# Optimization experiments

Hardware: AMD Instinct MI355X
Metric: run time of the kernel (lower is better)

The kernel has to match this reference:

```python
import jax, jax.numpy as jnp
import numpy as np

D_MODEL = 1024
N_HEAD = 16
T = 2048
HEAD = D_MODEL // N_HEAD  # 64
RANKS = [32, 16, 8, 8]
BLOCKS = [2048, 1024, 512, 256]  # seq_len // 2**i ('default')
OFFS = np.cumsum([0] + RANKS)


def setup_inputs() -> dict:
    key = jax.random.key(0)
    k0, k1, k2 = jax.random.split(key, 3)
    s = 0.02
    x = jax.random.normal(k0, (1, T, D_MODEL), dtype=jnp.float32)
    W_attn = jax.random.normal(k1, (D_MODEL, 3 * D_MODEL), dtype=jnp.float32) * s
    b_attn = jnp.zeros((3 * D_MODEL,), dtype=jnp.float32)
    W_proj = jax.random.normal(k2, (D_MODEL, D_MODEL), dtype=jnp.float32) * s
    b_proj = jnp.zeros((D_MODEL,), dtype=jnp.float32)
    return {"x": x, "W_attn": W_attn, "b_attn": b_attn, "W_proj": W_proj, "b_proj": b_proj}


def reference(x, W_attn, b_attn, W_proj, b_proj):
    B = x.shape[0]
    qkv = x @ W_attn + b_attn  # (B,T,3*D)
    q, k, v = jnp.split(qkv, 3, axis=-1)
    # (B,H,T,HEAD)
    q = q.reshape(B, T, N_HEAD, HEAD).transpose(0, 2, 1, 3)
    k = k.reshape(B, T, N_HEAD, HEAD).transpose(0, 2, 1, 3)
    v = v.reshape(B, T, N_HEAD, HEAD).transpose(0, 2, 1, 3)

    att = jnp.zeros((B, N_HEAD, T, T), dtype=x.dtype)
    for i, (bdx, r) in enumerate(zip(BLOCKS, RANKS)):
        nb = T // bdx
        qi = q[..., OFFS[i]:OFFS[i + 1]].reshape(B, N_HEAD, nb, bdx, r)
        ki = k[..., OFFS[i]:OFFS[i + 1]].reshape(B, N_HEAD, nb, bdx, r)
        blk = jnp.einsum('bhnir,bhnjr->bhnij', qi, ki) * (1.0 / r)  # (B,H,nb,bdx,bdx)
        # scatter block-diagonal scores into full T x T matrix
        att5 = att.reshape(B, N_HEAD, nb, bdx, nb, bdx)
        ar = jnp.arange(nb)
        att5 = att5.at[:, :, ar, :, ar, :].add(jnp.moveaxis(blk, 2, 0))
        att = att5.reshape(B, N_HEAD, T, T)

    causal = jnp.tril(jnp.ones((T, T), dtype=bool))
    att = jnp.where(causal, att, -jnp.inf)
    att = jax.nn.softmax(att, axis=-1)
    y = att @ v  # (B,H,T,HEAD)
    y = y.transpose(0, 2, 1, 3).reshape(B, T, D_MODEL)
    return y @ W_proj + b_proj
```

## Files before the change

### kernel.cpp

```cpp
#include <hip/hip_runtime.h>

using bf16x8 = __attribute__((ext_vector_type(8))) short;
using u16x8  = __attribute__((ext_vector_type(8))) unsigned short;
using f32x4  = __attribute__((ext_vector_type(4))) float;

#define DEVI __device__ __forceinline__

#define LOG2E 1.4426950408889634f

DEVI unsigned short f2bf(float f) {
  union { float ff; unsigned u; } v; v.ff = f;
  unsigned r = v.u + 0x7FFFu + ((v.u >> 16) & 1u);
  return (unsigned short)(r >> 16);
}

DEVI float bf2f(unsigned short s) {
  union { unsigned u; float f; } t; t.u = ((unsigned)s) << 16;
  return t.f;
}

DEVI int cvtpk(float lo, float hi) {
  int r;
  asm("v_cvt_pk_bf16_f32 %0, %1, %2" : "=v"(r) : "v"(lo), "v"(hi));
  return r;
}

DEVI void g2l16(const void* g, void* l) {
  __builtin_amdgcn_global_load_lds(
      (const __attribute__((address_space(1))) unsigned int*)g,
      (__attribute__((address_space(3))) unsigned int*)l, 16, 0, 0);
}

__global__ __launch_bounds__(256) void k_prep(
    const float* __restrict__ x, const float* __restrict__ Wa, const float* __restrict__ Wp,
    unsigned short* __restrict__ xb, unsigned short* __restrict__ WaT,
    unsigned short* __restrict__ WpT) {
  __shared__ unsigned short tile[32][33];
  const int b = blockIdx.x;
  const int tid = threadIdx.x;
  if (b < 2048) {
    const int i = b * 256 + tid;
    float4 v = reinterpret_cast<const float4*>(x)[i];
    ushort4 o;
    o.x = f2bf(v.x); o.y = f2bf(v.y); o.z = f2bf(v.z); o.w = f2bf(v.w);
    reinterpret_cast<ushort4*>(xb)[i] = o;
    return;
  }
  const float* in;
  unsigned short* out;
  int c0, r0, C;
  if (b < 5120) {
    const int bb = b - 2048;
    in = Wa; out = WaT; C = 3072;
    c0 = (bb % 96) * 32; r0 = (bb / 96) * 32;
  } else {
    const int bb = b - 5120;
    in = Wp; out = WpT; C = 1024;
    c0 = (bb & 31) * 32; r0 = (bb >> 5) * 32;
  }
  const int xx = tid & 31, yy = tid >> 5;
  for (int i = yy; i < 32; i += 8) tile[i][xx] = f2bf(in[(size_t)(r0 + i) * C + c0 + xx]);
  __syncthreads();
  for (int i = yy; i < 32; i += 8) out[(size_t)(c0 + i) * 1024 + r0 + xx] = tile[xx][i];
}

__global__ __launch_bounds__(256) void k_gemm_qkv(
    const unsigned short* __restrict__ A, const unsigned short* __restrict__ Bt,
    const float* __restrict__ bias,
    unsigned short* __restrict__ qs, unsigned short* __restrict__ kbuf,
    unsigned short* __restrict__ vT) {
  constexpr int K = 1024;
  __shared__ __align__(16) unsigned short As[2][128 * 64];
  __shared__ __align__(16) unsigned short Bs[2][64 * 64];
  const int lane = threadIdx.x & 63, wid = threadIdx.x >> 6;
  const int bx = blockIdx.x;
  const int nt = (bx & 7) * 6 + (bx >> 3);
  const int m0 = blockIdx.y * 128, n0 = nt * 64;
  const int wr = (wid >> 1) * 64, wc = (wid & 1) * 32;
  const int g = lane >> 4, li = lane & 15;
  f32x4 acc[4][2] = {};

#define STAGE_QKV(buf, k0)                                                              \
  {                                                                                     \
    _Pragma("unroll")                                                                   \
    for (int c = wid * 4; c < wid * 4 + 4; c++) {                                       \
      const int flat = c * 1024 + lane * 16;                                            \
      const int row = flat >> 7, colb = flat & 127;                                     \
      g2l16((const char*)A + ((size_t)(m0 + row) * K + (k0)) * 2 + colb,                \
            (char*)As[buf] + c * 1024);                                                 \
    }                                                                                   \
    _Pragma("unroll")                                                                   \
    for (int c = wid * 2; c < wid * 2 + 2; c++) {                                       \
      const int flat = c * 1024 + lane * 16;                                            \
      const int row = flat >> 7, colb = flat & 127;                                     \
      g2l16((const char*)Bt + ((size_t)(n0 + row) * K + (k0)) * 2 + colb,               \
            (char*)Bs[buf] + c * 1024);                                                 \
    }                                                                                   \
  }

  STAGE_QKV(0, 0);
  __syncthreads();
  int buf = 0;
  for (int t = 0; t < 16; t++) {
    if (t < 15) STAGE_QKV(buf ^ 1, (t + 1) * 64);
#pragma unroll
    for (int ks = 0; ks < 2; ks++) {
      const int kk = ks * 32 + g * 8;
      bf16x8 a[4], b[2];
#pragma unroll
      for (int i = 0; i < 4; i++)
        a[i] = *reinterpret_cast<const bf16x8*>(As[buf] + (wr + i * 16 + li) * 64 + kk);
#pragma unroll
      for (int j = 0; j < 2; j++)
        b[j] = *reinterpret_cast<const bf16x8*>(Bs[buf] + (wc + j * 16 + li) * 64 + kk);
#pragma unroll
      for (int i = 0; i < 4; i++)
#pragma unroll
        for (int j = 0; j < 2; j++)
          acc[i][j] = __builtin_amdgcn_mfma_f32_16x16x32_bf16(a[i], b[j], acc[i][j], 0, 0, 0);
    }
    __syncthreads();
    buf ^= 1;
  }

  const int rb = m0 + wr + g * 4;
  const int cb = n0 + wc + li;
  const int region = n0 >> 10;
  if (region == 0) {
#pragma unroll
    for (int j = 0; j < 2; j++) {
      const int c = cb + j * 16;
      const float bv = bias[c];
      const int hq = c >> 6, d = c & 63;
      const float sc = (d < 32 ? 0.03125f : (d < 48 ? 0.0625f : 0.125f)) * LOG2E;
#pragma unroll
      for (int i = 0; i < 4; i++)
#pragma unroll
        for (int r = 0; r < 4; r++)
          qs[((size_t)(hq * 2048 + rb + i * 16 + r) << 6) + d] = f2bf((acc[i][j][r] + bv) * sc);
    }
  } else if (region == 1) {
#pragma unroll
    for (int j = 0; j < 2; j++) {
      const int c = cb + j * 16;
      const float bv = bias[c];
      const int hq = (c >> 6) - 16, d = c & 63;
#pragma unroll
      for (int i = 0; i < 4; i++)
#pragma unroll
        for (int r = 0; r < 4; r++)
          kbuf[((size_t)(hq * 2048 + rb + i * 16 + r) << 6) + d] = f2bf(acc[i][j][r] + bv);
    }
  } else {
#pragma unroll
    for (int j = 0; j < 2; j++) {
      const int c = cb + j * 16;
      const float bv = bias[c];
      const int row = c - 2048;
#pragma unroll
      for (int i = 0; i < 4; i++) {
        const int t0 = rb + i * 16;
        ushort4 pk;
        pk.x = f2bf(acc[i][j][0] + bv);
        pk.y = f2bf(acc[i][j][1] + bv);
        pk.z = f2bf(acc[i][j][2] + bv);
        pk.w = f2bf(acc[i][j][3] + bv);
        *reinterpret_cast<ushort4*>(vT + (size_t)row * 2048 + t0) = pk;
      }
    }
  }
#undef STAGE_QKV
}

DEVI int chunk_off(int qt) {
  const int off[17] = {0,1,2,4,6,9,12,16,20,25,30,36,42,49,56,64,72};
  return off[qt];
}

__global__ __launch_bounds__(256) void k_attn_part(
    const unsigned short* __restrict__ qs, const unsigned short* __restrict__ kbuf,
    const unsigned short* __restrict__ vT,
    unsigned short* __restrict__ o_part, float* __restrict__ ml,
    unsigned short* __restrict__ yb) {
  __shared__ __align__(16) unsigned short Ks[2][128 * 64];
  __shared__ __align__(16) unsigned short Vs[2][64 * 128];
  const int lane = threadIdx.x & 63, wid = threadIdx.x >> 6;
  const int g = lane >> 4, li = lane & 15;

  const int h = blockIdx.x / 72;
  const int rem = blockIdx.x % 72;
  int qt = 0;
#pragma unroll
  for (int i = 0; i < 16; i++)
    if (rem >= chunk_off(i + 1)) qt = i + 1;
  const int ci = rem - chunk_off(qt);
  const int kt0 = ci * 2;
  const int kt1 = min(qt, kt0 + 1);
  const int q0 = qt * 128;

  const bf16x8 bzero = {0, 0, 0, 0, 0, 0, 0, 0};

#define STAGE_KV(buf, kt)                                                               \
  for (int c = wid; c < 16; c += 4) {                                                   \
    const int fb = c * 1024;                                                            \
    const int flat = fb + lane * 16;                                                    \
    {                                                                                   \
      const int row = flat >> 7;                                                        \
      const int cs = (((flat >> 4) & 7) ^ (row & 7)) << 4;                              \
      g2l16((const char*)kbuf + (((size_t)(h * 2048 + (kt) * 128 + row)) << 7) + cs,    \
            (char*)Ks[buf] + fb);                                                       \
    }                                                                                   \
    {                                                                                   \
      const int row = flat >> 8;                                                        \
      const int cs = (((flat >> 4) & 15) ^ (row & 15)) << 4;                            \
      g2l16((const char*)vT + ((size_t)(h * 64 + row) * 2048 + (kt) * 128) * 2 + cs,    \
            (char*)Vs[buf] + fb);                                                       \
    }                                                                                   \
  }

  STAGE_KV(0, kt0);
  if (kt1 > kt0) STAGE_KV(1, kt0 + 1);

  bf16x8 qf[2][2];
#pragma unroll
  for (int mi = 0; mi < 2; mi++)
#pragma unroll
    for (int ks = 0; ks < 2; ks++) {
      const int t = q0 + wid * 32 + mi * 16 + li;
      const int d = ks * 32 + g * 8;
      qf[mi][ks] = *reinterpret_cast<const bf16x8*>(qs + ((size_t)(h * 2048 + t) << 6) + d);
    }

  f32x4 o[2][4] = {};
  float m_run[2] = {-1e30f, -1e30f}, l_run[2] = {0.f, 0.f};

  const int q256 = qt >> 1;
  __syncthreads();

  int buf = 0;
  for (int kt = kt0; kt <= kt1; kt++) {
    const int x = q256 ^ (kt >> 1);
    const int Keff = (x == 0) ? 64 : ((x >= 4) ? 32 : ((x >= 2) ? 48 : 56));

    f32x4 st[8][2] = {};
    __builtin_amdgcn_s_setprio(1);
#pragma unroll
    for (int cf = 0; cf < 8; cf++) {
      const int krow = cf * 16 + li;
      const bf16x8 a0 = *reinterpret_cast<const bf16x8*>(
          Ks[buf] + krow * 64 + ((g ^ (krow & 7)) << 3));
      st[cf][0] = __builtin_amdgcn_mfma_f32_16x16x32_bf16(a0, qf[0][0], st[cf][0], 0, 0, 0);
      st[cf][1] = __builtin_amdgcn_mfma_f32_16x16x32_bf16(a0, qf[1][0], st[cf][1], 0, 0, 0);
    }
    if (Keff > 32) {
      const bool zf = (32 + g * 8) >= Keff;
#pragma unroll
      for (int cf = 0; cf < 8; cf++) {
        const int krow = cf * 16 + li;
        bf16x8 a1 = *reinterpret_cast<const bf16x8*>(
            Ks[buf] + krow * 64 + (((4 + g) ^ (krow & 7)) << 3));
        if (zf) a1 = bzero;
        st[cf][0] = __builtin_amdgcn_mfma_f32_16x16x32_bf16(a1, qf[0][1], st[cf][0], 0, 0, 0);
        st[cf][1] = __builtin_amdgcn_mfma_f32_16x16x32_bf16(a1, qf[1][1], st[cf][1], 0, 0, 0);
      }
    }
    __builtin_amdgcn_s_setprio(0);

    if (kt == qt) {
#pragma unroll
      for (int cf = 0; cf < 8; cf++)
#pragma unroll
        for (int mi = 0; mi < 2; mi++)
#pragma unroll
          for (int r = 0; r < 4; r++) {
            const int t2 = cf * 16 + g * 4 + r;
            const int qq = wid * 32 + mi * 16 + li;
            if (t2 > qq) st[cf][mi][r] = -1e30f;
          }
    }

    int pk[2][8][2];
#pragma unroll
    for (int mi = 0; mi < 2; mi++) {
      float c4[8];
#pragma unroll
      for (int cf = 0; cf < 8; cf++)
        c4[cf] = fmaxf(fmaxf(st[cf][mi][0], st[cf][mi][1]),
                       fmaxf(st[cf][mi][2], st[cf][mi][3]));
      const float ta = fmaxf(fmaxf(c4[0], c4[1]), fmaxf(c4[2], c4[3]));
      const float tb = fmaxf(fmaxf(c4[4], c4[5]), fmaxf(c4[6], c4[7]));
      float tm = fmaxf(ta, tb);
      tm = fmaxf(tm, __shfl_xor(tm, 16));
      tm = fmaxf(tm, __shfl_xor(tm, 32));
      if (!__all(tm <= m_run[mi] + 12.0f)) {
        const float mn = fmaxf(m_run[mi], tm);
        const float corr = exp2f(m_run[mi] - mn);
        m_run[mi] = mn;
        l_run[mi] *= corr;
        float cb0 = __shfl(corr, 4 * g + 0);
        float cb1 = __shfl(corr, 4 * g + 1);
        float cb2 = __shfl(corr, 4 * g + 2);
        float cb3 = __shfl(corr, 4 * g + 3);
#pragma unroll
        for (int nf = 0; nf < 4; nf++) {
          o[mi][nf][0] *= cb0; o[mi][nf][1] *= cb1;
          o[mi][nf][2] *= cb2; o[mi][nf][3] *= cb3;
        }
      }
      const float mn = m_run[mi];
      float sum = 0.f;
#pragma unroll
      for (int cf = 0; cf < 8; cf++) {
        const float p0 = exp2f(st[cf][mi][0] - mn);
        const float p1 = exp2f(st[cf][mi][1] - mn);
        const float p2 = exp2f(st[cf][mi][2] - mn);
        const float p3 = exp2f(st[cf][mi][3] - mn);
        sum += (p0 + p1) + (p2 + p3);
        pk[mi][cf][0] = cvtpk(p0, p1);
        pk[mi][cf][1] = cvtpk(p2, p3);
      }
      sum += __shfl_xor(sum, 16);
      sum += __shfl_xor(sum, 32);
      l_run[mi] += sum;
    }

    __builtin_amdgcn_s_setprio(1);
#pragma unroll
    for (int ks2 = 0; ks2 < 4; ks2++) {
      bf16x8 pa[2];
#pragma unroll
      for (int mi = 0; mi < 2; mi++) {
        union { int i[4]; bf16x8 v; } u;
        u.i[0] = pk[mi][2 * ks2][0];
        u.i[1] = pk[mi][2 * ks2][1];
        u.i[2] = pk[mi][2 * ks2 + 1][0];
        u.i[3] = pk[mi][2 * ks2 + 1][1];
        pa[mi] = u.v;
      }
      bf16x8 vb[4];
#pragma unroll
      for (int nf = 0; nf < 4; nf++) {
        const int vrow = nf * 16 + li;
        const int rm = vrow & 15;
        const int ch0 = 4 * ks2 + (g >> 1);
        const int b8 = (g & 1) * 8;
        union { struct { int2 lo, hi; } p; bf16x8 v; } u;
        u.p.lo = *reinterpret_cast<const int2*>(
            (const char*)Vs[buf] + vrow * 256 + (((ch0 + 0) ^ rm) << 4) + b8);
        u.p.hi = *reinterpret_cast<const int2*>(
            (const char*)Vs[buf] + vrow * 256 + (((ch0 + 2) ^ rm) << 4) + b8);
        vb[nf] = u.v;
      }
#pragma unroll
      for (int mi = 0; mi < 2; mi++)
#pragma unroll
        for (int nf = 0; nf < 4; nf++)
          o[mi][nf] = __builtin_amdgcn_mfma_f32_16x16x32_bf16(pa[mi], vb[nf], o[mi][nf], 0, 0, 0);
    }
    __builtin_amdgcn_s_setprio(0);
    buf ^= 1;
  }
#undef STAGE_KV

  if (qt < 2) {
#pragma unroll
    for (int mi = 0; mi < 2; mi++) {
      const float inv = 1.0f / l_run[mi];
      float ib[4];
      ib[0] = __shfl(inv, 4 * g + 0);
      ib[1] = __shfl(inv, 4 * g + 1);
      ib[2] = __shfl(inv, 4 * g + 2);
      ib[3] = __shfl(inv, 4 * g + 3);
#pragma unroll
      for (int nf = 0; nf < 4; nf++)
#pragma unroll
        for (int r = 0; r < 4; r++) {
          const int t = q0 + wid * 32 + mi * 16 + g * 4 + r;
          yb[(size_t)t * 1024 + h * 64 + nf * 16 + li] = f2bf(o[mi][nf][r] * ib[r]);
        }
    }
    return;
  }

  const size_t pbase = (size_t)blockIdx.x * 8192;
#pragma unroll
  for (int mi = 0; mi < 2; mi++) {
#pragma unroll
    for (int nf = 0; nf < 4; nf++)
#pragma unroll
      for (int r = 0; r < 4; r++) {
        const int row = wid * 32 + mi * 16 + g * 4 + r;
        o_part[pbase + (size_t)row * 64 + nf * 16 + li] = f2bf(o[mi][nf][r]);
      }
  }
  if (g == 0) {
#pragma unroll
    for (int mi = 0; mi < 2; mi++) {
      const int row = wid * 32 + mi * 16 + li;
      ml[(size_t)blockIdx.x * 256 + row] = m_run[mi];
      ml[(size_t)blockIdx.x * 256 + 128 + row] = l_run[mi];
    }
  }
}

__global__ __launch_bounds__(256) void k_combine(
    const unsigned short* __restrict__ o_part, const float* __restrict__ ml,
    unsigned short* __restrict__ yb) {
  const int h = blockIdx.x / 14, qt = blockIdx.x % 14 + 2;
  const int nc = (qt >> 1) + 1;
  const int base = h * 72 + chunk_off(qt);
  const int row = threadIdx.x >> 1;
  const int c0 = (threadIdx.x & 1) * 32;

  float M = -1e30f;
  for (int ci = 0; ci < nc; ci++)
    M = fmaxf(M, ml[(size_t)(base + ci) * 256 + row]);
  float L = 0.f;
  for (int ci = 0; ci < nc; ci++) {
    const float m = ml[(size_t)(base + ci) * 256 + row];
    const float l = ml[(size_t)(base + ci) * 256 + 128 + row];
    L += exp2f(m - M) * l;
  }
  const float inv = 1.0f / L;

  float acc[32];
#pragma unroll
  for (int j = 0; j < 32; j++) acc[j] = 0.f;
  for (int ci = 0; ci < nc; ci++) {
    const float wc = exp2f(ml[(size_t)(base + ci) * 256 + row] - M);
    const u16x8* src = reinterpret_cast<const u16x8*>(
        o_part + (size_t)(base + ci) * 8192 + (size_t)row * 64 + c0);
#pragma unroll
    for (int j8 = 0; j8 < 4; j8++) {
      u16x8 v = src[j8];
#pragma unroll
      for (int e = 0; e < 8; e++) acc[j8 * 8 + e] += wc * bf2f(v[e]);
    }
  }
  const int t = qt * 128 + row;
  unsigned short* dst = yb + (size_t)t * 1024 + h * 64 + c0;
#pragma unroll
  for (int j8 = 0; j8 < 4; j8++) {
    ushort4 pk;
    pk.x = f2bf(acc[j8 * 8 + 0] * inv);
    pk.y = f2bf(acc[j8 * 8 + 1] * inv);
    pk.z = f2bf(acc[j8 * 8 + 2] * inv);
    pk.w = f2bf(acc[j8 * 8 + 3] * inv);
    ushort4 pk2;
    pk2.x = f2bf(acc[j8 * 8 + 4] * inv);
    pk2.y = f2bf(acc[j8 * 8 + 5] * inv);
    pk2.z = f2bf(acc[j8 * 8 + 6] * inv);
    pk2.w = f2bf(acc[j8 * 8 + 7] * inv);
    reinterpret_cast<ushort4*>(dst)[j8 * 2 + 0] = pk;
    reinterpret_cast<ushort4*>(dst)[j8 * 2 + 1] = pk2;
  }
}

__global__ __launch_bounds__(256) void k_gemm_proj(
    const unsigned short* __restrict__ A, const unsigned short* __restrict__ Bt,
    const float* __restrict__ bias, float* __restrict__ out) {
  constexpr int K = 1024;
  __shared__ __align__(16) unsigned short As[2][64 * 64];
  __shared__ __align__(16) unsigned short Bs[2][64 * 64];
  const int lane = threadIdx.x & 63, wid = threadIdx.x >> 6;
  const int bx = blockIdx.x;
  const int nt = (bx & 7) * 2 + (bx >> 3);
  const int m0 = blockIdx.y * 64, n0 = nt * 64;
  const int wr = (wid >> 1) * 32, wc = (wid & 1) * 32;
  const int g = lane >> 4, li = lane & 15;
  f32x4 acc[2][2] = {};

#define STAGE_PROJ(buf, k0)                                                             \
  {                                                                                     \
    _Pragma("unroll")                                                                   \
    for (int c = wid * 2; c < wid * 2 + 2; c++) {                                       \
      const int flat = c * 1024 + lane * 16;                                            \
      const int row = flat >> 7, colb = flat & 127;                                     \
      g2l16((const char*)A + ((size_t)(m0 + row) * K + (k0)) * 2 + colb,                \
            (char*)As[buf] + c * 1024);                                                 \
      g2l16((const char*)Bt + ((size_t)(n0 + row) * K + (k0)) * 2 + colb,               \
            (char*)Bs[buf] + c * 1024);                                                 \
    }                                                                                   \
  }

  STAGE_PROJ(0, 0);
  __syncthreads();
  int buf = 0;
  for (int t = 0; t < 16; t++) {
    if (t < 15) STAGE_PROJ(buf ^ 1, (t + 1) * 64);
#pragma unroll
    for (int ks = 0; ks < 2; ks++) {
      const int kk = ks * 32 + g * 8;
      bf16x8 a[2], b[2];
#pragma unroll
      for (int i = 0; i < 2; i++)
        a[i] = *reinterpret_cast<const bf16x8*>(As[buf] + (wr + i * 16 + li) * 64 + kk);
#pragma unroll
      for (int j = 0; j < 2; j++)
        b[j] = *reinterpret_cast<const bf16x8*>(Bs[buf] + (wc + j * 16 + li) * 64 + kk);
#pragma unroll
      for (int i = 0; i < 2; i++)
#pragma unroll
        for (int j = 0; j < 2; j++)
          acc[i][j] = __builtin_amdgcn_mfma_f32_16x16x32_bf16(a[i], b[j], acc[i][j], 0, 0, 0);
    }
    __syncthreads();
    buf ^= 1;
  }

  const int rb = m0 + wr + g * 4;
  const int cb = n0 + wc + li;
#pragma unroll
  for (int j = 0; j < 2; j++) {
    const int c = cb + j * 16;
    const float bv = bias[c];
#pragma unroll
    for (int i = 0; i < 2; i++) {
#pragma unroll
      for (int r = 0; r < 4; r++) {
        const int t = rb + i * 16 + r;
        out[(size_t)t * 1024 + c] = acc[i][j][r] + bv;
      }
    }
  }
#undef STAGE_PROJ
}

extern "C" void kernel_launch(void* const* d_in, const int* in_sizes, int n_in,
                              void* d_out, int out_size, void* d_ws, size_t ws_size,
                              hipStream_t stream) {
  const float* x      = (const float*)d_in[0];
  const float* W_attn = (const float*)d_in[1];
  const float* b_attn = (const float*)d_in[2];
  const float* W_proj = (const float*)d_in[3];
  const float* b_proj = (const float*)d_in[4];
  float* out = (float*)d_out;
  char* ws = (char*)d_ws;
  const size_t MB = 1024 * 1024;
  unsigned short* xb  = (unsigned short*)(ws + 0 * MB);
  unsigned short* WaT = (unsigned short*)(ws + 4 * MB);
  unsigned short* WpT = (unsigned short*)(ws + 10 * MB);
  unsigned short* qs  = (unsigned short*)(ws + 12 * MB);
  unsigned short* kb  = (unsigned short*)(ws + 16 * MB);
  unsigned short* vT  = (unsigned short*)(ws + 20 * MB);
  unsigned short* yb  = (unsigned short*)(ws + 24 * MB);
  unsigned short* o_part = (unsigned short*)(ws + 28 * MB);
  float* ml     = (float*)(ws + 48 * MB);

  k_prep<<<dim3(6144), dim3(256), 0, stream>>>(x, W_attn, W_proj, xb, WaT, WpT);
  k_gemm_qkv<<<dim3(48, 16), dim3(256), 0, stream>>>(xb, WaT, b_attn, qs, kb, vT);
  k_attn_part<<<dim3(1152), dim3(256), 0, stream>>>(qs, kb, vT, o_part, ml, yb);
  k_combine<<<dim3(224), dim3(256), 0, stream>>>(o_part, ml, yb);
  k_gemm_proj<<<dim3(16, 32), dim3(256), 0, stream>>>(yb, WpT, b_proj, out);
}
```

Baseline: 97.00 us.

## Fuse all stages into one cooperative persistent kernel with grid syncs

Replaces the five separate kernel launches with a single cooperative persistent kernel that loops over each stage's jobs and separates stages with grid-wide syncs, keeping the old launches only as a fallback. This removes launch gaps and per-launch overhead. The QKV GEMM tile changes from 128x64 to 128x96, and the projection GEMM tiling is also changed. Risks are grid sync cost, fewer resident blocks than jobs so each block runs several jobs in sequence, and larger LDS per block lowering occupancy.

Result: slower. 276.6 us (+185.1%).

```diff
diff --git a/kernel.cpp b/kernel.cpp
--- a/kernel.cpp
+++ b/kernel.cpp
@@ -1,11 +1,13 @@
 #include <hip/hip_runtime.h>
+#include <hip/hip_cooperative_groups.h>
+
+namespace cg = cooperative_groups;
 
 using bf16x8 = __attribute__((ext_vector_type(8))) short;
 using u16x8  = __attribute__((ext_vector_type(8))) unsigned short;
 using f32x4  = __attribute__((ext_vector_type(4))) float;
 
 #define DEVI __device__ __forceinline__
-
 #define LOG2E 1.4426950408889634f
 
 DEVI unsigned short f2bf(float f) {
@@ -31,15 +33,17 @@
       (__attribute__((address_space(3))) unsigned int*)l, 16, 0, 0);
 }
 
-__global__ __launch_bounds__(256) void k_prep(
-    const float* __restrict__ x, const float* __restrict__ Wa, const float* __restrict__ Wp,
-    unsigned short* __restrict__ xb, unsigned short* __restrict__ WaT,
-    unsigned short* __restrict__ WpT) {
-  __shared__ unsigned short tile[32][33];
-  const int b = blockIdx.x;
-  const int tid = threadIdx.x;
-  if (b < 2048) {
-    const int i = b * 256 + tid;
+DEVI int chunk_off(int qt) {
+  const int off[17] = {0,1,2,4,6,9,12,16,20,25,30,36,42,49,56,64,72};
+  return off[qt];
+}
+
+
+DEVI void prep_job(int j, int tid, unsigned short (*tile)[33],
+                   const float* x, const float* Wa, const float* Wp,
+                   unsigned short* xb, unsigned short* WaT, unsigned short* WpT) {
+  if (j < 2048) {
+    const int i = j * 256 + tid;
     float4 v = reinterpret_cast<const float4*>(x)[i];
     ushort4 o;
     o.x = f2bf(v.x); o.y = f2bf(v.y); o.z = f2bf(v.z); o.w = f2bf(v.w);
@@ -47,57 +51,55 @@
     return;
   }
   const float* in;
-  unsigned short* out;
+  unsigned short* outp;
   int c0, r0, C;
-  if (b < 5120) {
-    const int bb = b - 2048;
-    in = Wa; out = WaT; C = 3072;
+  if (j < 5120) {
+    const int bb = j - 2048;
+    in = Wa; outp = WaT; C = 3072;
     c0 = (bb % 96) * 32; r0 = (bb / 96) * 32;
   } else {
-    const int bb = b - 5120;
-    in = Wp; out = WpT; C = 1024;
+    const int bb = j - 5120;
+    in = Wp; outp = WpT; C = 1024;
     c0 = (bb & 31) * 32; r0 = (bb >> 5) * 32;
   }
   const int xx = tid & 31, yy = tid >> 5;
+  __syncthreads();
   for (int i = yy; i < 32; i += 8) tile[i][xx] = f2bf(in[(size_t)(r0 + i) * C + c0 + xx]);
   __syncthreads();
-  for (int i = yy; i < 32; i += 8) out[(size_t)(c0 + i) * 1024 + r0 + xx] = tile[xx][i];
-}
-
-__global__ __launch_bounds__(256) void k_gemm_qkv(
-    const unsigned short* __restrict__ A, const unsigned short* __restrict__ Bt,
-    const float* __restrict__ bias,
-    unsigned short* __restrict__ qs, unsigned short* __restrict__ kbuf,
-    unsigned short* __restrict__ vT) {
+  for (int i = yy; i < 32; i += 8) outp[(size_t)(c0 + i) * 1024 + r0 + xx] = tile[xx][i];
+}
+
+DEVI void qkv_job(int j, int lane, int wid, int g, int li,
+                  unsigned short (*SA)[8192], unsigned short (*SB)[8192],
+                  const unsigned short* xb, const unsigned short* WaT,
+                  const float* b_attn, unsigned short* qs,
+                  unsigned short* kbuf, unsigned short* vT) {
+  const int nt = (j & 7) * 4 + ((j >> 3) & 3);
+  const int mt = j >> 5;
+  const int m0 = mt * 128, n0 = nt * 96;
+  const int wr = (wid >> 1) * 64, wc = (wid & 1) * 48;
   constexpr int K = 1024;
-  __shared__ __align__(16) unsigned short As[2][128 * 64];
-  __shared__ __align__(16) unsigned short Bs[2][64 * 64];
-  const int lane = threadIdx.x & 63, wid = threadIdx.x >> 6;
-  const int bx = blockIdx.x;
-  const int nt = (bx & 7) * 6 + (bx >> 3);
-  const int m0 = blockIdx.y * 128, n0 = nt * 64;
-  const int wr = (wid >> 1) * 64, wc = (wid & 1) * 32;
-  const int g = lane >> 4, li = lane & 15;
-  f32x4 acc[4][2] = {};
-
-#define STAGE_QKV(buf, k0)                                                              \
-  {                                                                                     \
-    _Pragma("unroll")                                                                   \
-    for (int c = wid * 4; c < wid * 4 + 4; c++) {                                       \
-      const int flat = c * 1024 + lane * 16;                                            \
-      const int row = flat >> 7, colb = flat & 127;                                     \
-      g2l16((const char*)A + ((size_t)(m0 + row) * K + (k0)) * 2 + colb,                \
-            (char*)As[buf] + c * 1024);                                                 \
-    }                                                                                   \
-    _Pragma("unroll")                                                                   \
-    for (int c = wid * 2; c < wid * 2 + 2; c++) {                                       \
-      const int flat = c * 1024 + lane * 16;                                            \
-      const int row = flat >> 7, colb = flat & 127;                                     \
-      g2l16((const char*)Bt + ((size_t)(n0 + row) * K + (k0)) * 2 + colb,               \
-            (char*)Bs[buf] + c * 1024);                                                 \
-    }                                                                                   \
-  }
-
+  f32x4 acc[4][3] = {};
+
+#define STAGE_QKV(buf, k0)                                                            \
+  {                                                                                   \
+    _Pragma("unroll")                                                                 \
+    for (int c = wid * 4; c < wid * 4 + 4; c++) {                                     \
+      const int flat = c * 1024 + lane * 16;                                          \
+      const int row = flat >> 7, colb = flat & 127;                                   \
+      g2l16((const char*)xb + ((size_t)(m0 + row) * K + (k0)) * 2 + colb,             \
+            (char*)SA[buf] + c * 1024);                                               \
+    }                                                                                 \
+    _Pragma("unroll")                                                                 \
+    for (int c = wid * 3; c < wid * 3 + 3; c++) {                                     \
+      const int flat = c * 1024 + lane * 16;                                          \
+      const int row = flat >> 7, colb = flat & 127;                                   \
+      g2l16((const char*)WaT + ((size_t)(n0 + row) * K + (k0)) * 2 + colb,            \
+            (char*)SB[buf] + c * 1024);                                               \
+    }                                                                                 \
+  }
+
+  __syncthreads();
   STAGE_QKV(0, 0);
   __syncthreads();
   int buf = 0;
@@ -106,89 +108,70 @@
 #pragma unroll
     for (int ks = 0; ks < 2; ks++) {
       const int kk = ks * 32 + g * 8;
-      bf16x8 a[4], b[2];
+      bf16x8 a[4], b[3];
 #pragma unroll
       for (int i = 0; i < 4; i++)
-        a[i] = *reinterpret_cast<const bf16x8*>(As[buf] + (wr + i * 16 + li) * 64 + kk);
-#pragma unroll
-      for (int j = 0; j < 2; j++)
-        b[j] = *reinterpret_cast<const bf16x8*>(Bs[buf] + (wc + j * 16 + li) * 64 + kk);
+        a[i] = *reinterpret_cast<const bf16x8*>(SA[buf] + (wr + i * 16 + li) * 64 + kk);
+#pragma unroll
+      for (int jj = 0; jj < 3; jj++)
+        b[jj] = *reinterpret_cast<const bf16x8*>(SB[buf] + (wc + jj * 16 + li) * 64 + kk);
 #pragma unroll
       for (int i = 0; i < 4; i++)
 #pragma unroll
-        for (int j = 0; j < 2; j++)
-          acc[i][j] = __builtin_amdgcn_mfma_f32_16x16x32_bf16(a[i], b[j], acc[i][j], 0, 0, 0);
+        for (int jj = 0; jj < 3; jj++)
+          acc[i][jj] = __builtin_amdgcn_mfma_f32_16x16x32_bf16(a[i], b[jj], acc[i][jj], 0, 0, 0);
     }
     __syncthreads();
     buf ^= 1;
   }
+#undef STAGE_QKV
 
   const int rb = m0 + wr + g * 4;
-  const int cb = n0 + wc + li;
-  const int region = n0 >> 10;
-  if (region == 0) {
-#pragma unroll
-    for (int j = 0; j < 2; j++) {
-      const int c = cb + j * 16;
-      const float bv = bias[c];
+#pragma unroll
+  for (int jj = 0; jj < 3; jj++) {
+    const int cfb = n0 + wc + jj * 16;
+    const int c = cfb + li;
+    const int region = cfb >> 10;
+    const float bv = b_attn[c];
+    if (region == 0) {
       const int hq = c >> 6, d = c & 63;
       const float sc = (d < 32 ? 0.03125f : (d < 48 ? 0.0625f : 0.125f)) * LOG2E;
 #pragma unroll
       for (int i = 0; i < 4; i++)
 #pragma unroll
         for (int r = 0; r < 4; r++)
-          qs[((size_t)(hq * 2048 + rb + i * 16 + r) << 6) + d] = f2bf((acc[i][j][r] + bv) * sc);
-    }
-  } else if (region == 1) {
-#pragma unroll
-    for (int j = 0; j < 2; j++) {
-      const int c = cb + j * 16;
-      const float bv = bias[c];
+          qs[((size_t)(hq * 2048 + rb + i * 16 + r) << 6) + d] =
+              f2bf((acc[i][jj][r] + bv) * sc);
+    } else if (region == 1) {
       const int hq = (c >> 6) - 16, d = c & 63;
 #pragma unroll
       for (int i = 0; i < 4; i++)
 #pragma unroll
         for (int r = 0; r < 4; r++)
-          kbuf[((size_t)(hq * 2048 + rb + i * 16 + r) << 6) + d] = f2bf(acc[i][j][r] + bv);
-    }
-  } else {
-#pragma unroll
-    for (int j = 0; j < 2; j++) {
-      const int c = cb + j * 16;
-      const float bv = bias[c];
+          kbuf[((size_t)(hq * 2048 + rb + i * 16 + r) << 6) + d] =
+              f2bf(acc[i][jj][r] + bv);
+    } else {
       const int row = c - 2048;
 #pragma unroll
       for (int i = 0; i < 4; i++) {
-        const int t0 = rb + i * 16;
         ushort4 pk;
-        pk.x = f2bf(acc[i][j][0] + bv);
-        pk.y = f2bf(acc[i][j][1] + bv);
-        pk.z = f2bf(acc[i][j][2] + bv);
-        pk.w = f2bf(acc[i][j][3] + bv);
-        *reinterpret_cast<ushort4*>(vT + (size_t)row * 2048 + t0) = pk;
+        pk.x = f2bf(acc[i][jj][0] + bv);
+        pk.y = f2bf(acc[i][jj][1] + bv);
+        pk.z = f2bf(acc[i][jj][2] + bv);
+        pk.w = f2bf(acc[i][jj][3] + bv);
+        *reinterpret_cast<ushort4*>(vT + (size_t)row * 2048 + rb + i * 16) = pk;
       }
     }
   }
-#undef STAGE_QKV
-}
-
-DEVI int chunk_off(int qt) {
-  const int off[17] = {0,1,2,4,6,9,12,16,20,25,30,36,42,49,56,64,72};
-  return off[qt];
-}
-
-__global__ __launch_bounds__(256) void k_attn_part(
-    const unsigned short* __restrict__ qs, const unsigned short* __restrict__ kbuf,
-    const unsigned short* __restrict__ vT,
-    unsigned short* __restrict__ o_part, float* __restrict__ ml,
-    unsigned short* __restrict__ yb) {
-  __shared__ __align__(16) unsigned short Ks[2][128 * 64];
-  __shared__ __align__(16) unsigned short Vs[2][64 * 128];
-  const int lane = threadIdx.x & 63, wid = threadIdx.x >> 6;
-  const int g = lane >> 4, li = lane & 15;
-
-  const int h = blockIdx.x / 72;
-  const int rem = blockIdx.x % 72;
+}
+
+DEVI void attn_job(int j, int lane, int wid, int g, int li,
+                   unsigned short (*SA)[8192], unsigned short (*SB)[8192],
+                   const unsigned short* qs, const unsigned short* kbuf,
+                   const unsigned short* vT, unsigned short* o_part,
+                   float* ml, unsigned short* yb) {
+  const int h = j / 72;
+  const int rem = j % 72;
   int qt = 0;
 #pragma unroll
   for (int i = 0; i < 16; i++)
@@ -197,27 +180,27 @@
   const int kt0 = ci * 2;
   const int kt1 = min(qt, kt0 + 1);
   const int q0 = qt * 128;
-
   const bf16x8 bzero = {0, 0, 0, 0, 0, 0, 0, 0};
 
-#define STAGE_KV(buf, kt)                                                               \
-  for (int c = wid; c < 16; c += 4) {                                                   \
-    const int fb = c * 1024;                                                            \
-    const int flat = fb + lane * 16;                                                    \
-    {                                                                                   \
-      const int row = flat >> 7;                                                        \
-      const int cs = (((flat >> 4) & 7) ^ (row & 7)) << 4;                              \
-      g2l16((const char*)kbuf + (((size_t)(h * 2048 + (kt) * 128 + row)) << 7) + cs,    \
-            (char*)Ks[buf] + fb);                                                       \
-    }                                                                                   \
-    {                                                                                   \
-      const int row = flat >> 8;                                                        \
-      const int cs = (((flat >> 4) & 15) ^ (row & 15)) << 4;                            \
-      g2l16((const char*)vT + ((size_t)(h * 64 + row) * 2048 + (kt) * 128) * 2 + cs,    \
-            (char*)Vs[buf] + fb);                                                       \
-    }                                                                                   \
-  }
-
+#define STAGE_KV(buf, kt)                                                             \
+  for (int c = wid; c < 16; c += 4) {                                                 \
+    const int fb = c * 1024;                                                          \
+    const int flat = fb + lane * 16;                                                  \
+    {                                                                                 \
+      const int row = flat >> 7;                                                      \
+      const int cs = (((flat >> 4) & 7) ^ (row & 7)) << 4;                            \
+      g2l16((const char*)kbuf + (((size_t)(h * 2048 + (kt) * 128 + row)) << 7) + cs,  \
+            (char*)SA[buf] + fb);                                                     \
+    }                                                                                 \
+    {                                                                                 \
+      const int row = flat >> 8;                                                      \
+      const int cs = (((flat >> 4) & 15) ^ (row & 15)) << 4;                          \
+      g2l16((const char*)vT + ((size_t)(h * 64 + row) * 2048 + (kt) * 128) * 2 + cs,  \
+            (char*)SB[buf] + fb);                                                     \
+    }                                                                                 \
+  }
+
+  __syncthreads();
   STAGE_KV(0, kt0);
   if (kt1 > kt0) STAGE_KV(1, kt0 + 1);
 
@@ -233,14 +216,13 @@
 
   f32x4 o[2][4] = {};
   float m_run[2] = {-1e30f, -1e30f}, l_run[2] = {0.f, 0.f};
-
   const int q256 = qt >> 1;
   __syncthreads();
 
   int buf = 0;
   for (int kt = kt0; kt <= kt1; kt++) {
-    const int x = q256 ^ (kt >> 1);
-    const int Keff = (x == 0) ? 64 : ((x >= 4) ? 32 : ((x >= 2) ? 48 : 56));
+    const int xx = q256 ^ (kt >> 1);
+    const int Keff = (xx == 0) ? 64 : ((xx >= 4) ? 32 : ((xx >= 2) ? 48 : 56));
 
     f32x4 st[8][2] = {};
     __builtin_amdgcn_s_setprio(1);
@@ -248,7 +230,7 @@
     for (int cf = 0; cf < 8; cf++) {
       const int krow = cf * 16 + li;
       const bf16x8 a0 = *reinterpret_cast<const bf16x8*>(
-          Ks[buf] + krow * 64 + ((g ^ (krow & 7)) << 3));
+          SA[buf] + krow * 64 + ((g ^ (krow & 7)) << 3));
       st[cf][0] = __builtin_amdgcn_mfma_f32_16x16x32_bf16(a0, qf[0][0], st[cf][0], 0, 0, 0);
       st[cf][1] = __builtin_amdgcn_mfma_f32_16x16x32_bf16(a0, qf[1][0], st[cf][1], 0, 0, 0);
     }
@@ -258,7 +240,7 @@
       for (int cf = 0; cf < 8; cf++) {
         const int krow = cf * 16 + li;
         bf16x8 a1 = *reinterpret_cast<const bf16x8*>(
-            Ks[buf] + krow * 64 + (((4 + g) ^ (krow & 7)) << 3));
+            SA[buf] + krow * 64 + (((4 + g) ^ (krow & 7)) << 3));
         if (zf) a1 = bzero;
         st[cf][0] = __builtin_amdgcn_mfma_f32_16x16x32_bf16(a1, qf[0][1], st[cf][0], 0, 0, 0);
         st[cf][1] = __builtin_amdgcn_mfma_f32_16x16x32_bf16(a1, qf[1][1], st[cf][1], 0, 0, 0);
@@ -346,9 +328,9 @@
         const int b8 = (g & 1) * 8;
         union { struct { int2 lo, hi; } p; bf16x8 v; } u;
         u.p.lo = *reinterpret_cast<const int2*>(
-            (const char*)Vs[buf] + vrow * 256 + (((ch0 + 0) ^ rm) << 4) + b8);
+            (const char*)SB[buf] + vrow * 256 + (((ch0 + 0) ^ rm) << 4) + b8);
         u.p.hi = *reinterpret_cast<const int2*>(
-            (const char*)Vs[buf] + vrow * 256 + (((ch0 + 2) ^ rm) << 4) + b8);
+            (const char*)SB[buf] + vrow * 256 + (((ch0 + 2) ^ rm) << 4) + b8);
         vb[nf] = u.v;
       }
 #pragma unroll
@@ -382,9 +364,9 @@
     return;
   }
 
-  const size_t pbase = (size_t)blockIdx.x * 8192;
-#pragma unroll
-  for (int mi = 0; mi < 2; mi++) {
+  const size_t pbase = (size_t)j * 8192;
+#pragma unroll
+  for (int mi = 0; mi < 2; mi++)
 #pragma unroll
     for (int nf = 0; nf < 4; nf++)
 #pragma unroll
@@ -392,25 +374,24 @@
         const int row = wid * 32 + mi * 16 + g * 4 + r;
         o_part[pbase + (size_t)row * 64 + nf * 16 + li] = f2bf(o[mi][nf][r]);
       }
-  }
   if (g == 0) {
 #pragma unroll
     for (int mi = 0; mi < 2; mi++) {
       const int row = wid * 32 + mi * 16 + li;
-      ml[(size_t)blockIdx.x * 256 + row] = m_run[mi];
-      ml[(size_t)blockIdx.x * 256 + 128 + row] = l_run[mi];
-    }
-  }
-}
-
-__global__ __launch_bounds__(256) void k_combine(
-    const unsigned short* __restrict__ o_part, const float* __restrict__ ml,
-    unsigned short* __restrict__ yb) {
-  const int h = blockIdx.x / 14, qt = blockIdx.x % 14 + 2;
+      ml[(size_t)j * 256 + row] = m_run[mi];
+      ml[(size_t)j * 256 + 128 + row] = l_run[mi];
+    }
+  }
+}
+
+DEVI void combine_job(int j, int tid,
+                      const unsigned short* o_part, const float* ml,
+                      unsigned short* yb) {
+  const int h = j / 14, qt = j % 14 + 2;
   const int nc = (qt >> 1) + 1;
   const int base = h * 72 + chunk_off(qt);
-  const int row = threadIdx.x >> 1;
-  const int c0 = (threadIdx.x & 1) * 32;
+  const int row = tid >> 1;
+  const int c0 = (tid & 1) * 32;
 
   float M = -1e30f;
   for (int ci = 0; ci < nc; ci++)
@@ -425,7 +406,7 @@
 
   float acc[32];
 #pragma unroll
-  for (int j = 0; j < 32; j++) acc[j] = 0.f;
+  for (int jj = 0; jj < 32; jj++) acc[jj] = 0.f;
   for (int ci = 0; ci < nc; ci++) {
     const float wc = exp2f(ml[(size_t)(base + ci) * 256 + row] - M);
     const u16x8* src = reinterpret_cast<const u16x8*>(
@@ -456,74 +437,150 @@
   }
 }
 
+DEVI void proj_job(int j, int lane, int wid, int g, int li,
+                   unsigned short (*SA)[8192], unsigned short (*SB)[8192],
+                   const unsigned short* yb, const unsigned short* WpT,
+                   const float* b_proj, float* out) {
+  const int nt = (j & 7) * 2 + ((j >> 3) & 1);
+  const int mt = j >> 4;
+  const int m0 = mt * 64, n0 = nt * 64;
+  const int wr = (wid >> 1) * 32, wc = (wid & 1) * 32;
+  constexpr int K = 1024;
+  f32x4 acc[2][2] = {};
+
+#define STAGE_PROJ(buf, k0)                                                           \
+  {                                                                                   \
+    _Pragma("unroll")                                                                 \
+    for (int c = wid * 2; c < wid * 2 + 2; c++) {                                     \
+      const int flat = c * 1024 + lane * 16;                                          \
+      const int row = flat >> 7, colb = flat & 127;                                   \
+      g2l16((const char*)yb + ((size_t)(m0 + row) * K + (k0)) * 2 + colb,             \
+            (char*)SA[buf] + c * 1024);                                               \
+      g2l16((const char*)WpT + ((size_t)(n0 + row) * K + (k0)) * 2 + colb,            \
+            (char*)SB[buf] + c * 1024);                                               \
+    }                                                                                 \
+  }
+
+  __syncthreads();
+  STAGE_PROJ(0, 0);
+  __syncthreads();
+  int buf = 0;
+  for (int t = 0; t < 16; t++) {
+    if (t < 15) STAGE_PROJ(buf ^ 1, (t + 1) * 64);
+#pragma unroll
+    for (int ks = 0; ks < 2; ks++) {
+      const int kk = ks * 32 + g * 8;
+      bf16x8 a[2], b[2];
+#pragma unroll
+      for (int i = 0; i < 2; i++)
+        a[i] = *reinterpret_cast<const bf16x8*>(SA[buf] + (wr + i * 16 + li) * 64 + kk);
+#pragma unroll
+      for (int jj = 0; jj < 2; jj++)
+        b[jj] = *reinterpret_cast<const bf16x8*>(SB[buf] + (wc + jj * 16 + li) * 64 + kk);
+#pragma unroll
+      for (int i = 0; i < 2; i++)
+#pragma unroll
+        for (int jj = 0; jj < 2; jj++)
+          acc[i][jj] = __builtin_amdgcn_mfma_f32_16x16x32_bf16(a[i], b[jj], acc[i][jj], 0, 0, 0);
+    }
+    __syncthreads();
+    buf ^= 1;
+  }
+#undef STAGE_PROJ
+
+  const int rb = m0 + wr + g * 4;
+  const int cb = n0 + wc + li;
+#pragma unroll
+  for (int jj = 0; jj < 2; jj++) {
+    const int c = cb + jj * 16;
+    const float bv = b_proj[c];
+#pragma unroll
+    for (int i = 0; i < 2; i++)
+#pragma unroll
+      for (int r = 0; r < 4; r++)
+        out[(size_t)(rb + i * 16 + r) * 1024 + c] = acc[i][jj][r] + bv;
+  }
+}
+
+__global__ __launch_bounds__(256, 2) void k_mega(
+    const float* __restrict__ x, const float* __restrict__ Wa,
+    const float* __restrict__ b_attn, const float* __restrict__ Wp,
+    const float* __restrict__ b_proj, float* __restrict__ out,
+    unsigned short* __restrict__ xb, unsigned short* __restrict__ WaT,
+    unsigned short* __restrict__ WpT, unsigned short* __restrict__ qs,
+    unsigned short* __restrict__ kbuf, unsigned short* __restrict__ vT,
+    unsigned short* __restrict__ yb, unsigned short* __restrict__ o_part,
+    float* __restrict__ ml) {
+  __shared__ __align__(16) unsigned short SA[2][8192];
+  __shared__ __align__(16) unsigned short SB[2][8192];
+  cg::grid_group grid = cg::this_grid();
+
+  const int nb = gridDim.x;
+  const int bid = blockIdx.x;
+  const int tid = threadIdx.x;
+  const int lane = tid & 63, wid = tid >> 6;
+  const int g = lane >> 4, li = lane & 15;
+  unsigned short (*tile)[33] = reinterpret_cast<unsigned short (*)[33]>(&SA[0][0]);
+
+  for (int j = bid; j < 6144; j += nb)
+    prep_job(j, tid, tile, x, Wa, Wp, xb, WaT, WpT);
+  grid.sync();
+  for (int j = bid; j < 512; j += nb)
+    qkv_job(j, lane, wid, g, li, SA, SB, xb, WaT, b_attn, qs, kbuf, vT);
+  grid.sync();
+  for (int j = bid; j < 1152; j += nb)
+    attn_job(j, lane, wid, g, li, SA, SB, qs, kbuf, vT, o_part, ml, yb);
+  grid.sync();
+  for (int j = bid; j < 224; j += nb)
+    combine_job(j, tid, o_part, ml, yb);
+  grid.sync();
+  for (int j = bid; j < 512; j += nb)
+    proj_job(j, lane, wid, g, li, SA, SB, yb, WpT, b_proj, out);
+}
+
+__global__ __launch_bounds__(256) void k_prep(
+    const float* __restrict__ x, const float* __restrict__ Wa, const float* __restrict__ Wp,
+    unsigned short* __restrict__ xb, unsigned short* __restrict__ WaT,
+    unsigned short* __restrict__ WpT) {
+  __shared__ unsigned short tile[32][33];
+  prep_job(blockIdx.x, threadIdx.x, tile, x, Wa, Wp, xb, WaT, WpT);
+}
+
+__global__ __launch_bounds__(256) void k_gemm_qkv(
+    const unsigned short* __restrict__ A, const unsigned short* __restrict__ Bt,
+    const float* __restrict__ bias,
+    unsigned short* __restrict__ qs, unsigned short* __restrict__ kbuf,
+    unsigned short* __restrict__ vT) {
+  __shared__ __align__(16) unsigned short SA[2][8192];
+  __shared__ __align__(16) unsigned short SB[2][8192];
+  const int lane = threadIdx.x & 63, wid = threadIdx.x >> 6;
+  qkv_job(blockIdx.x, lane, wid, lane >> 4, lane & 15, SA, SB, A, Bt, bias, qs, kbuf, vT);
+}
+
+__global__ __launch_bounds__(256) void k_attn_part(
+    const unsigned short* __restrict__ qs, const unsigned short* __restrict__ kbuf,
+    const unsigned short* __restrict__ vT,
+    unsigned short* __restrict__ o_part, float* __restrict__ ml,
+    unsigned short* __restrict__ yb) {
+  __shared__ __align__(16) unsigned short SA[2][8192];
+  __shared__ __align__(16) unsigned short SB[2][8192];
+  const int lane = threadIdx.x & 63, wid = threadIdx.x >> 6;
+  attn_job(blockIdx.x, lane, wid, lane >> 4, lane & 15, SA, SB, qs, kbuf, vT, o_part, ml, yb);
+}
+
+__global__ __launch_bounds__(256) void k_combine(
+    const unsigned short* __restrict__ o_part, const float* __restrict__ ml,
+    unsigned short* __restrict__ yb) {
+  combine_job(blockIdx.x, threadIdx.x, o_part, ml, yb);
+}
+
 __global__ __launch_bounds__(256) void k_gemm_proj(
     const unsigned short* __restrict__ A, const unsigned short* __restrict__ Bt,
     const float* __restrict__ bias, float* __restrict__ out) {
-  constexpr int K = 1024;
-  __shared__ __align__(16) unsigned short As[2][64 * 64];
-  __shared__ __align__(16) unsigned short Bs[2][64 * 64];
+  __shared__ __align__(16) unsigned short SA[2][8192];
+  __shared__ __align__(16) unsigned short SB[2][8192];
   const int lane = threadIdx.x & 63, wid = threadIdx.x >> 6;
-  const int bx = blockIdx.x;
-  const int nt = (bx & 7) * 2 + (bx >> 3);
-  const int m0 = blockIdx.y * 64, n0 = nt * 64;
-  const int wr = (wid >> 1) * 32, wc = (wid & 1) * 32;
-  const int g = lane >> 4, li = lane & 15;
-  f32x4 acc[2][2] = {};
-
-#define STAGE_PROJ(buf, k0)                                                             \
-  {                                                                                     \
-    _Pragma("unroll")                                                                   \
-    for (int c = wid * 2; c < wid * 2 + 2; c++) {                                       \
-      const int flat = c * 1024 + lane * 16;                                            \
-      const int row = flat >> 7, colb = flat & 127;                                     \
-      g2l16((const char*)A + ((size_t)(m0 + row) * K + (k0)) * 2 + colb,                \
-            (char*)As[buf] + c * 1024);                                                 \
-      g2l16((const char*)Bt + ((size_t)(n0 + row) * K + (k0)) * 2 + colb,               \
-            (char*)Bs[buf] + c * 1024);                                                 \
-    }                                                                                   \
-  }
-
-  STAGE_PROJ(0, 0);
-  __syncthreads();
-  int buf = 0;
-  for (int t = 0; t < 16; t++) {
-    if (t < 15) STAGE_PROJ(buf ^ 1, (t + 1) * 64);
-#pragma unroll
-    for (int ks = 0; ks < 2; ks++) {
-      const int kk = ks * 32 + g * 8;
-      bf16x8 a[2], b[2];
-#pragma unroll
-      for (int i = 0; i < 2; i++)
-        a[i] = *reinterpret_cast<const bf16x8*>(As[buf] + (wr + i * 16 + li) * 64 + kk);
-#pragma unroll
-      for (int j = 0; j < 2; j++)
-        b[j] = *reinterpret_cast<const bf16x8*>(Bs[buf] + (wc + j * 16 + li) * 64 + kk);
-#pragma unroll
-      for (int i = 0; i < 2; i++)
-#pragma unroll
-        for (int j = 0; j < 2; j++)
-          acc[i][j] = __builtin_amdgcn_mfma_f32_16x16x32_bf16(a[i], b[j], acc[i][j], 0, 0, 0);
-    }
-    __syncthreads();
-    buf ^= 1;
-  }
-
-  const int rb = m0 + wr + g * 4;
-  const int cb = n0 + wc + li;
-#pragma unroll
-  for (int j = 0; j < 2; j++) {
-    const int c = cb + j * 16;
-    const float bv = bias[c];
-#pragma unroll
-    for (int i = 0; i < 2; i++) {
-#pragma unroll
-      for (int r = 0; r < 4; r++) {
-        const int t = rb + i * 16 + r;
-        out[(size_t)t * 1024 + c] = acc[i][j][r] + bv;
-      }
-    }
-  }
-#undef STAGE_PROJ
+  proj_job(blockIdx.x, lane, wid, lane >> 4, lane & 15, SA, SB, A, Bt, bias, out);
 }
 
 extern "C" void kernel_launch(void* const* d_in, const int* in_sizes, int n_in,
@@ -547,9 +604,27 @@
   unsigned short* o_part = (unsigned short*)(ws + 28 * MB);
   float* ml     = (float*)(ws + 48 * MB);
 
-  k_prep<<<dim3(6144), dim3(256), 0, stream>>>(x, W_attn, W_proj, xb, WaT, WpT);
-  k_gemm_qkv<<<dim3(48, 16), dim3(256), 0, stream>>>(xb, WaT, b_attn, qs, kb, vT);
-  k_attn_part<<<dim3(1152), dim3(256), 0, stream>>>(qs, kb, vT, o_part, ml, yb);
-  k_combine<<<dim3(224), dim3(256), 0, stream>>>(o_part, ml, yb);
-  k_gemm_proj<<<dim3(16, 32), dim3(256), 0, stream>>>(yb, WpT, b_proj, out);
-}
+  int maxBpc = 0;
+  hipError_t qe = hipOccupancyMaxActiveBlocksPerMultiprocessor(&maxBpc, (const void*)k_mega, 256, 0);
+  int gridN = 512;
+  if (qe == hipSuccess && maxBpc >= 1) {
+    int cap = maxBpc * 256;
+    if (cap < gridN) gridN = cap;
+  }
+  const float* xa = x; const float* wa = W_attn; const float* ba = b_attn;
+  const float* wp = W_proj; const float* bp = b_proj; float* oo = out;
+  void* args[] = {
+    (void*)&xa, (void*)&wa, (void*)&ba, (void*)&wp, (void*)&bp,
+    (void*)&oo, (void*)&xb, (void*)&WaT, (void*)&WpT, (void*)&qs,
+    (void*)&kb, (void*)&vT, (void*)&yb, (void*)&o_part, (void*)&ml
+  };
+  hipError_t e = hipLaunchCooperativeKernel((void*)k_mega, dim3(gridN), dim3(256), args, 0, stream);
+  if (e != hipSuccess) {
+    (void)hipGetLastError();
+    k_prep<<<dim3(6144), dim3(256), 0, stream>>>(x, W_attn, W_proj, xb, WaT, WpT);
+    k_gemm_qkv<<<dim3(512), dim3(256), 0, stream>>>(xb, WaT, b_attn, qs, kb, vT);
+    k_attn_part<<<dim3(1152), dim3(256), 0, stream>>>(qs, kb, vT, o_part, ml, yb);
+    k_combine<<<dim3(224), dim3(256), 0, stream>>>(o_part, ml, yb);
+    k_gemm_proj<<<dim3(512), dim3(256), 0, stream>>>(yb, WpT, b_proj, out);
+  }
+}
```

## Drop LDS staging in attention kernel and read K/V directly from global memory

Applied to the files above, without the earlier changes.

The attention partial kernel no longer copies K and V tiles into double-buffered shared memory. It loads MFMA operands straight from global memory, relying on the caches. The mi loop now wraps the whole score/softmax/PV sequence to cut live registers, and launch bounds request 4 blocks per CU for more occupancy. This removes LDS traffic and the barrier, but each of the four waves now reads the same K/V data from global/L2 separately, using narrow, strided accesses (8-byte V reads with a 2048-element row stride).

After: 214.3 us. +121.0%, slower.

```diff
diff --git a/kernel.cpp b/kernel.cpp
--- a/kernel.cpp
+++ b/kernel.cpp
@@ -5,7 +5,6 @@
 using f32x4  = __attribute__((ext_vector_type(4))) float;
 
 #define DEVI __device__ __forceinline__
-
 #define LOG2E 1.4426950408889634f
 
 DEVI unsigned short f2bf(float f) {
@@ -177,13 +176,11 @@
   return off[qt];
 }
 
-__global__ __launch_bounds__(256) void k_attn_part(
+__global__ __launch_bounds__(256, 4) void k_attn_part(
     const unsigned short* __restrict__ qs, const unsigned short* __restrict__ kbuf,
     const unsigned short* __restrict__ vT,
     unsigned short* __restrict__ o_part, float* __restrict__ ml,
     unsigned short* __restrict__ yb) {
-  __shared__ __align__(16) unsigned short Ks[2][128 * 64];
-  __shared__ __align__(16) unsigned short Vs[2][64 * 128];
   const int lane = threadIdx.x & 63, wid = threadIdx.x >> 6;
   const int g = lane >> 4, li = lane & 15;
 
@@ -197,29 +194,7 @@
   const int kt0 = ci * 2;
   const int kt1 = min(qt, kt0 + 1);
   const int q0 = qt * 128;
-
   const bf16x8 bzero = {0, 0, 0, 0, 0, 0, 0, 0};
-
-#define STAGE_KV(buf, kt)                                                               \
-  for (int c = wid; c < 16; c += 4) {                                                   \
-    const int fb = c * 1024;                                                            \
-    const int flat = fb + lane * 16;                                                    \
-    {                                                                                   \
-      const int row = flat >> 7;                                                        \
-      const int cs = (((flat >> 4) & 7) ^ (row & 7)) << 4;                              \
-      g2l16((const char*)kbuf + (((size_t)(h * 2048 + (kt) * 128 + row)) << 7) + cs,    \
-            (char*)Ks[buf] + fb);                                                       \
-    }                                                                                   \
-    {                                                                                   \
-      const int row = flat >> 8;                                                        \
-      const int cs = (((flat >> 4) & 15) ^ (row & 15)) << 4;                            \
-      g2l16((const char*)vT + ((size_t)(h * 64 + row) * 2048 + (kt) * 128) * 2 + cs,    \
-            (char*)Vs[buf] + fb);                                                       \
-    }                                                                                   \
-  }
-
-  STAGE_KV(0, kt0);
-  if (kt1 > kt0) STAGE_KV(1, kt0 + 1);
 
   bf16x8 qf[2][2];
 #pragma unroll
@@ -233,60 +208,54 @@
 
   f32x4 o[2][4] = {};
   float m_run[2] = {-1e30f, -1e30f}, l_run[2] = {0.f, 0.f};
-
   const int q256 = qt >> 1;
-  __syncthreads();
-
-  int buf = 0;
+
+  const unsigned short* Kb = kbuf + ((size_t)h * 2048) * 64;
+  const unsigned short* Vb = vT + (size_t)h * 64 * 2048;
+
   for (int kt = kt0; kt <= kt1; kt++) {
-    const int x = q256 ^ (kt >> 1);
-    const int Keff = (x == 0) ? 64 : ((x >= 4) ? 32 : ((x >= 2) ? 48 : 56));
-
-    f32x4 st[8][2] = {};
-    __builtin_amdgcn_s_setprio(1);
-#pragma unroll
-    for (int cf = 0; cf < 8; cf++) {
-      const int krow = cf * 16 + li;
-      const bf16x8 a0 = *reinterpret_cast<const bf16x8*>(
-          Ks[buf] + krow * 64 + ((g ^ (krow & 7)) << 3));
-      st[cf][0] = __builtin_amdgcn_mfma_f32_16x16x32_bf16(a0, qf[0][0], st[cf][0], 0, 0, 0);
-      st[cf][1] = __builtin_amdgcn_mfma_f32_16x16x32_bf16(a0, qf[1][0], st[cf][1], 0, 0, 0);
-    }
-    if (Keff > 32) {
-      const bool zf = (32 + g * 8) >= Keff;
+    const int xx = q256 ^ (kt >> 1);
+    const int Keff = (xx == 0) ? 64 : ((xx >= 4) ? 32 : ((xx >= 2) ? 48 : 56));
+    const unsigned short* Kt = Kb + (size_t)(kt * 128) * 64;
+    const unsigned short* Vt = Vb + kt * 128;
+
+#pragma unroll
+    for (int mi = 0; mi < 2; mi++) {
+      f32x4 st[8] = {};
+      __builtin_amdgcn_s_setprio(1);
 #pragma unroll
       for (int cf = 0; cf < 8; cf++) {
         const int krow = cf * 16 + li;
-        bf16x8 a1 = *reinterpret_cast<const bf16x8*>(
-            Ks[buf] + krow * 64 + (((4 + g) ^ (krow & 7)) << 3));
-        if (zf) a1 = bzero;
-        st[cf][0] = __builtin_amdgcn_mfma_f32_16x16x32_bf16(a1, qf[0][1], st[cf][0], 0, 0, 0);
-        st[cf][1] = __builtin_amdgcn_mfma_f32_16x16x32_bf16(a1, qf[1][1], st[cf][1], 0, 0, 0);
-      }
-    }
-    __builtin_amdgcn_s_setprio(0);
-
-    if (kt == qt) {
-#pragma unroll
-      for (int cf = 0; cf < 8; cf++)
-#pragma unroll
-        for (int mi = 0; mi < 2; mi++)
+        const bf16x8 a0 = *reinterpret_cast<const bf16x8*>(Kt + krow * 64 + g * 8);
+        st[cf] = __builtin_amdgcn_mfma_f32_16x16x32_bf16(a0, qf[mi][0], st[cf], 0, 0, 0);
+      }
+      if (Keff > 32) {
+        const bool zf = (32 + g * 8) >= Keff;
+#pragma unroll
+        for (int cf = 0; cf < 8; cf++) {
+          const int krow = cf * 16 + li;
+          bf16x8 a1 = *reinterpret_cast<const bf16x8*>(Kt + krow * 64 + 32 + g * 8);
+          if (zf) a1 = bzero;
+          st[cf] = __builtin_amdgcn_mfma_f32_16x16x32_bf16(a1, qf[mi][1], st[cf], 0, 0, 0);
+        }
+      }
+      __builtin_amdgcn_s_setprio(0);
+
+      if (kt == qt) {
+#pragma unroll
+        for (int cf = 0; cf < 8; cf++)
 #pragma unroll
           for (int r = 0; r < 4; r++) {
             const int t2 = cf * 16 + g * 4 + r;
             const int qq = wid * 32 + mi * 16 + li;
-            if (t2 > qq) st[cf][mi][r] = -1e30f;
+            if (t2 > qq) st[cf][r] = -1e30f;
           }
-    }
-
-    int pk[2][8][2];
-#pragma unroll
-    for (int mi = 0; mi < 2; mi++) {
+      }
+
       float c4[8];
 #pragma unroll
       for (int cf = 0; cf < 8; cf++)
-        c4[cf] = fmaxf(fmaxf(st[cf][mi][0], st[cf][mi][1]),
-                       fmaxf(st[cf][mi][2], st[cf][mi][3]));
+        c4[cf] = fmaxf(fmaxf(st[cf][0], st[cf][1]), fmaxf(st[cf][2], st[cf][3]));
       const float ta = fmaxf(fmaxf(c4[0], c4[1]), fmaxf(c4[2], c4[3]));
       const float tb = fmaxf(fmaxf(c4[4], c4[5]), fmaxf(c4[6], c4[7]));
       float tm = fmaxf(ta, tb);
@@ -308,59 +277,48 @@
         }
       }
       const float mn = m_run[mi];
+      int pk[8][2];
       float sum = 0.f;
 #pragma unroll
       for (int cf = 0; cf < 8; cf++) {
-        const float p0 = exp2f(st[cf][mi][0] - mn);
-        const float p1 = exp2f(st[cf][mi][1] - mn);
-        const float p2 = exp2f(st[cf][mi][2] - mn);
-        const float p3 = exp2f(st[cf][mi][3] - mn);
+        const float p0 = exp2f(st[cf][0] - mn);
+        const float p1 = exp2f(st[cf][1] - mn);
+        const float p2 = exp2f(st[cf][2] - mn);
+        const float p3 = exp2f(st[cf][3] - mn);
         sum += (p0 + p1) + (p2 + p3);
-        pk[mi][cf][0] = cvtpk(p0, p1);
-        pk[mi][cf][1] = cvtpk(p2, p3);
+        pk[cf][0] = cvtpk(p0, p1);
+        pk[cf][1] = cvtpk(p2, p3);
       }
       sum += __shfl_xor(sum, 16);
       sum += __shfl_xor(sum, 32);
       l_run[mi] += sum;
-    }
-
-    __builtin_amdgcn_s_setprio(1);
-#pragma unroll
-    for (int ks2 = 0; ks2 < 4; ks2++) {
-      bf16x8 pa[2];
-#pragma unroll
-      for (int mi = 0; mi < 2; mi++) {
-        union { int i[4]; bf16x8 v; } u;
-        u.i[0] = pk[mi][2 * ks2][0];
-        u.i[1] = pk[mi][2 * ks2][1];
-        u.i[2] = pk[mi][2 * ks2 + 1][0];
-        u.i[3] = pk[mi][2 * ks2 + 1][1];
-        pa[mi] = u.v;
-      }
-      bf16x8 vb[4];
-#pragma unroll
-      for (int nf = 0; nf < 4; nf++) {
-        const int vrow = nf * 16 + li;
-        const int rm = vrow & 15;
-        const int ch0 = 4 * ks2 + (g >> 1);
-        const int b8 = (g & 1) * 8;
-        union { struct { int2 lo, hi; } p; bf16x8 v; } u;
-        u.p.lo = *reinterpret_cast<const int2*>(
-            (const char*)Vs[buf] + vrow * 256 + (((ch0 + 0) ^ rm) << 4) + b8);
-        u.p.hi = *reinterpret_cast<const int2*>(
-            (const char*)Vs[buf] + vrow * 256 + (((ch0 + 2) ^ rm) << 4) + b8);
-        vb[nf] = u.v;
-      }
-#pragma unroll
-      for (int mi = 0; mi < 2; mi++)
+
+      __builtin_amdgcn_s_setprio(1);
+#pragma unroll
+      for (int ks2 = 0; ks2 < 4; ks2++) {
+        union { int i[4]; bf16x8 v; } up;
+        up.i[0] = pk[2 * ks2][0];
+        up.i[1] = pk[2 * ks2][1];
+        up.i[2] = pk[2 * ks2 + 1][0];
+        up.i[3] = pk[2 * ks2 + 1][1];
+        const bf16x8 pa = up.v;
+        bf16x8 vb[4];
+#pragma unroll
+        for (int nf = 0; nf < 4; nf++) {
+          const int vrow = nf * 16 + li;
+          const unsigned short* vp = Vt + (size_t)vrow * 2048 + 32 * ks2 + 4 * g;
+          union { struct { int2 lo, hi; } p; bf16x8 v; } u;
+          u.p.lo = *reinterpret_cast<const int2*>(vp);
+          u.p.hi = *reinterpret_cast<const int2*>(vp + 16);
+          vb[nf] = u.v;
+        }
 #pragma unroll
         for (int nf = 0; nf < 4; nf++)
-          o[mi][nf] = __builtin_amdgcn_mfma_f32_16x16x32_bf16(pa[mi], vb[nf], o[mi][nf], 0, 0, 0);
-    }
-    __builtin_amdgcn_s_setprio(0);
-    buf ^= 1;
-  }
-#undef STAGE_KV
+          o[mi][nf] = __builtin_amdgcn_mfma_f32_16x16x32_bf16(pa, vb[nf], o[mi][nf], 0, 0, 0);
+      }
+      __builtin_amdgcn_s_setprio(0);
+    }
+  }
 
   if (qt < 2) {
 #pragma unroll
@@ -384,7 +342,7 @@
 
   const size_t pbase = (size_t)blockIdx.x * 8192;
 #pragma unroll
-  for (int mi = 0; mi < 2; mi++) {
+  for (int mi = 0; mi < 2; mi++)
 #pragma unroll
     for (int nf = 0; nf < 4; nf++)
 #pragma unroll
@@ -392,7 +350,6 @@
         const int row = wid * 32 + mi * 16 + g * 4 + r;
         o_part[pbase + (size_t)row * 64 + nf * 16 + li] = f2bf(o[mi][nf][r]);
       }
-  }
   if (g == 0) {
 #pragma unroll
     for (int mi = 0; mi < 2; mi++) {
```
